# Kernel optimization log

Hardware: AMD Instinct MI355X
Metric: run time of the kernel (lower is better)

Reference implementation:

```python
import jax, jax.numpy as jnp
import numpy as np

G, B, I, H = 512, 64, 32, 64  # num_of_grids, batch, input_size, hidden_size


def setup_inputs() -> dict:
    key = jax.random.key(0)
    ks = jax.random.split(key, 13)
    s = lambda *sh: 1.0 / np.sqrt(sh[-1])
    return {
        "input_data": jax.random.normal(ks[0], (G, B, I), jnp.float32),
        "h0": jax.random.normal(ks[1], (B, H), jnp.float32),
        "c0": jax.random.normal(ks[2], (B, H), jnp.float32),
        # LSTMCell params (torch layout: gates ordered i, f, g, o)
        "W_ih": jax.random.uniform(ks[3], (4 * H, I), jnp.float32, -s(H), s(H)),
        "W_hh": jax.random.uniform(ks[4], (4 * H, H), jnp.float32, -s(H), s(H)),
        "b_ih": jax.random.uniform(ks[5], (4 * H,), jnp.float32, -s(H), s(H)),
        "b_hh": jax.random.uniform(ks[6], (4 * H,), jnp.float32, -s(H), s(H)),
        # MLP head: H*G -> 10*G -> 5*G -> G
        "W1": jax.random.uniform(ks[7], (10 * G, H * G), jnp.float32, -s(H * G), s(H * G)),
        "b1": jax.random.uniform(ks[8], (10 * G,), jnp.float32, -s(H * G), s(H * G)),
        "W2": jax.random.uniform(ks[9], (5 * G, 10 * G), jnp.float32, -s(10 * G), s(10 * G)),
        "b2": jax.random.uniform(ks[10], (5 * G,), jnp.float32, -s(10 * G), s(10 * G)),
        "W3": jax.random.uniform(ks[11], (G, 5 * G), jnp.float32, -s(5 * G), s(5 * G)),
        "b3": jax.random.uniform(ks[12], (G,), jnp.float32, -s(5 * G), s(5 * G)),
    }


def reference(input_data, h0, c0, W_ih, W_hh, b_ih, b_hh, W1, b1, W2, b2, W3, b3):
    def step(carry, x):
        h, c = carry
        gates = x @ W_ih.T + b_ih + h @ W_hh.T + b_hh  # [B, 4H]
        i, f, g, o = jnp.split(gates, 4, axis=-1)
        i, f, o = jax.nn.sigmoid(i), jax.nn.sigmoid(f), jax.nn.sigmoid(o)
        g = jnp.tanh(g)
        c = f * c + i * g
        h = o * jnp.tanh(c)
        return (h, c), h

    _, hs = jax.lax.scan(step, (h0, c0), input_data)  # [G, B, H]
    # torch.cat(list, dim=1) over grid order -> [B, G*H]
    out_all = jnp.transpose(hs, (1, 0, 2)).reshape(h0.shape[0], -1)
    x = out_all @ W1.T + b1
    x = x @ W2.T + b2
    x = x @ W3.T + b3
    return jax.nn.sigmoid(x)  # [B, G]
```

## Files before the change

kernel.cpp:

```cpp
#include <hip/hip_runtime.h>
#include <hip/hip_fp16.h>

#define G_ 512
#define B_ 64
#define I_ 32
#define H_ 64
#define NGATE 256

typedef _Float16 half8 __attribute__((ext_vector_type(8)));
typedef _Float16 h4 __attribute__((ext_vector_type(4)));
typedef _Float16 h2 __attribute__((ext_vector_type(2)));
typedef float f32x4 __attribute__((ext_vector_type(4)));

#if __has_builtin(__builtin_amdgcn_fdot2)
#define FDOT2(a, b, c) __builtin_amdgcn_fdot2((a), (b), (c), false)
#else
#define FDOT2(a, b, c) ((c) + (float)(a)[0] * (float)(b)[0] + (float)(a)[1] * (float)(b)[1])
#endif

__device__ __forceinline__ float sigf(float x) {
  return 1.0f / (1.0f + __expf(-x));
}
__device__ __forceinline__ float tanh_fast(float x) {
  x = fminf(fmaxf(x, -15.0f), 15.0f);
  float e = __expf(2.0f * x);
  return (e - 1.0f) / (e + 1.0f);
}

__global__ __launch_bounds__(256) void k_xproj(
    const float* __restrict__ input, const float* __restrict__ W_ih,
    const float* __restrict__ b_ih, const float* __restrict__ b_hh,
    _Float16* __restrict__ xproj) {
  const int g = blockIdx.x;
  const int t = threadIdx.x;
  const int col = t >> 2;
  const int q = t & 3;
  const int row = q * H_ + col;
  __shared__ alignas(16) float inp[B_ * I_];
  const float* ing = input + (size_t)g * (B_ * I_);
#pragma unroll
  for (int u = 0; u < (B_ * I_) / 256; ++u) inp[u * 256 + t] = ing[u * 256 + t];
  float w[I_];
#pragma unroll
  for (int k = 0; k < I_; k += 4) {
    f32x4 v = *(const f32x4*)(W_ih + (size_t)row * I_ + k);
    w[k] = v[0]; w[k + 1] = v[1]; w[k + 2] = v[2]; w[k + 3] = v[3];
  }
  const float bias = b_ih[row] + b_hh[row];
  __syncthreads();
  for (int b = 0; b < B_; ++b) {
    float a0 = bias, a1 = 0.f, a2 = 0.f, a3 = 0.f;
#pragma unroll
    for (int k = 0; k < I_; k += 4) {
      f32x4 iv = *(const f32x4*)&inp[b * I_ + k];
      a0 += iv[0] * w[k]; a1 += iv[1] * w[k + 1];
      a2 += iv[2] * w[k + 2]; a3 += iv[3] * w[k + 3];
    }
    xproj[((size_t)b * G_ + g) * NGATE + t] = (_Float16)((a0 + a1) + (a2 + a3));
  }
}

__device__ __forceinline__ void scan_row(
    int b, int j, const _Float16* __restrict__ xproj,
    const float* __restrict__ h0, const float* __restrict__ c0,
    const float* __restrict__ W_hh, _Float16* __restrict__ hs,
    _Float16* hsh) {
  h2 w[4][32];
#pragma unroll
  for (int q = 0; q < 4; ++q) {
    const f32x4* wr = (const f32x4*)(W_hh + (size_t)(q * H_ + j) * H_);
#pragma unroll
    for (int kk = 0; kk < 16; ++kk) {
      f32x4 v = wr[kk];
      h2 t0, t1;
      t0[0] = (_Float16)v[0]; t0[1] = (_Float16)v[1];
      t1[0] = (_Float16)v[2]; t1[1] = (_Float16)v[3];
      w[2 * kk & 0 ? 0 : 0][0] = w[0][0];
      w[q][2 * kk] = t0;
      w[q][2 * kk + 1] = t1;
    }
  }
  float c = c0[b * H_ + j];
  hsh[j] = (_Float16)h0[b * H_ + j];

  const h4* xrow = (const h4*)(xproj + (size_t)b * G_ * NGATE) + j;
  h4 p[8];
#pragma unroll
  for (int d = 0; d < 8; ++d) p[d] = xrow[(size_t)d * 64];

  _Float16* hrow = hs + (size_t)b * (G_ * H_) + j;

  for (int g0 = 0; g0 < G_; g0 += 8) {
#pragma unroll
    for (int d = 0; d < 8; ++d) {
      const int g = g0 + d;
      float a[4], a2[4];
#pragma unroll
      for (int q = 0; q < 4; ++q) { a[q] = (float)p[d][q]; a2[q] = 0.0f; }
      const f32x4* hp4 = (const f32x4*)hsh;
#pragma unroll
      for (int k4 = 0; k4 < 4; ++k4) {
        f32x4 hv4 = hp4[k4];
#pragma unroll
        for (int t = 0; t < 4; ++t) {
          h2 hv = __builtin_bit_cast(h2, hv4[t]);
#pragma unroll
          for (int q = 0; q < 4; ++q) a[q] = FDOT2(hv, w[q][k4 * 4 + t], a[q]);
        }
      }
#pragma unroll
      for (int k4 = 4; k4 < 8; ++k4) {
        f32x4 hv4 = hp4[k4];
#pragma unroll
        for (int t = 0; t < 4; ++t) {
          h2 hv = __builtin_bit_cast(h2, hv4[t]);
#pragma unroll
          for (int q = 0; q < 4; ++q) a2[q] = FDOT2(hv, w[q][k4 * 4 + t], a2[q]);
        }
      }
#pragma unroll
      for (int q = 0; q < 4; ++q) a[q] += a2[q];

      float ig = sigf(a[0]);
      float fg = sigf(a[1]);
      float gg = tanh_fast(a[2]);
      float og = sigf(a[3]);
      c = fg * c + ig * gg;
      float hh = og * tanh_fast(c);
      _Float16 hf = (_Float16)hh;
      hsh[j] = hf;
      hrow[(size_t)g * H_] = hf;
      if (g + 8 < G_) p[d] = xrow[(size_t)(g + 8) * 64];
    }
  }
}

__device__ __forceinline__ void conv_loop(
    const float* __restrict__ src, _Float16* __restrict__ dst, int nvec,
    int gtid, int gstride) {
  for (int i = gtid; i < nvec; i += gstride) {
    const f32x4* s = (const f32x4*)(src + (size_t)i * 8);
    f32x4 v0 = s[0];
    f32x4 v1 = s[1];
    half8 h;
    h[0] = (_Float16)v0[0]; h[1] = (_Float16)v0[1];
    h[2] = (_Float16)v0[2]; h[3] = (_Float16)v0[3];
    h[4] = (_Float16)v1[0]; h[5] = (_Float16)v1[1];
    h[6] = (_Float16)v1[2]; h[7] = (_Float16)v1[3];
    *(half8*)(dst + (size_t)i * 8) = h;
  }
}

#define NCONV 2048

__global__ __launch_bounds__(256) void k_scan_conv(
    const _Float16* __restrict__ xproj, const float* __restrict__ h0,
    const float* __restrict__ c0, const float* __restrict__ W_hh,
    _Float16* __restrict__ hs,
    const float* __restrict__ W1, _Float16* __restrict__ W1h,
    const float* __restrict__ W2, _Float16* __restrict__ W2h,
    const float* __restrict__ W3, _Float16* __restrict__ W3h) {
  __shared__ alignas(16) _Float16 hsh[H_];
  const int bid = blockIdx.x;
  if (bid < B_) {
    if (threadIdx.x < 64)
      scan_row(bid, threadIdx.x, xproj, h0, c0, W_hh, hs, hsh);
    return;
  }
  const int gtid = (bid - B_) * 256 + threadIdx.x;
  const int gstride = NCONV * 256;
  conv_loop(W1, W1h, (5120 * 32768) / 8, gtid, gstride);
  conv_loop(W2, W2h, (2560 * 5120) / 8, gtid, gstride);
  conv_loop(W3, W3h, (512 * 2560) / 8, gtid, gstride);
}

template <int N, int K, int KC, int NTILES, int KW>
__global__ __launch_bounds__(256) void k_gemm_h(
    const _Float16* __restrict__ X, const _Float16* __restrict__ Wh,
    float* __restrict__ part) {
  constexpr int ROWB = KW * 2;
  constexpr int SLOTS = ROWB / 16;
  constexpr int RPP = 64 / SLOTS;
  constexpr int NPASS = 16 / RPP;
  static_assert(KC % KW == 0, "stage divisibility");
  __shared__ alignas(16) _Float16 wl[64 * KW];
  const int bid = blockIdx.x;
  const int n0 = (bid % NTILES) * 64;
  const int ks = bid / NTILES;
  const int kbeg = ks * KC;
  const int lane = threadIdx.x & 63;
  const int wave = threadIdx.x >> 6;
  const int r = lane & 15;
  const int gq = lane >> 4;
  const int s = lane % SLOTS;
  const int ro = lane / SLOTS;

  const _Float16* xrow = X + (size_t)r * K + kbeg + 8 * gq;
  f32x4 acc[4] = {};

  for (int st = 0; st < KC / KW; ++st) {
    const int kst = kbeg + st * KW;
#pragma unroll
    for (int pass = 0; pass < NPASS; ++pass) {
      const int rr = wave * 16 + pass * RPP + ro;
      half8 hv = *(const half8*)(Wh + (size_t)(n0 + rr) * K + kst + s * 8);
      int byte = rr * ROWB + s * 16;
      byte ^= (rr & 7) << 4;
      *(half8*)((char*)wl + byte) = hv;
    }
    __syncthreads();
#pragma unroll
    for (int k32 = 0; k32 < KW; k32 += 32) {
      int rbyte = (wave * 16 + r) * ROWB + (k32 + 8 * gq) * 2;
      rbyte ^= (r & 7) << 4;
      half8 bfv = *(const half8*)((const char*)wl + rbyte);
      const _Float16* xp = xrow + st * KW + k32;
#pragma unroll
      for (int mi = 0; mi < 4; ++mi) {
        half8 af = *(const half8*)(xp + (size_t)(mi * 16) * K);
        acc[mi] = __builtin_amdgcn_mfma_f32_16x16x32_f16(af, bfv, acc[mi], 0, 0, 0);
      }
    }
    __syncthreads();
  }
#pragma unroll
  for (int mi = 0; mi < 4; ++mi) {
#pragma unroll
    for (int q = 0; q < 4; ++q) {
      int row = mi * 16 + gq * 4 + q;
      part[((size_t)ks * 64 + row) * N + n0 + wave * 16 + r] = acc[mi][q];
    }
  }
}

template <int N, int KS>
__global__ __launch_bounds__(256) void k_reduce(
    const float* __restrict__ part, const float* __restrict__ bias,
    _Float16* __restrict__ out) {
  const int idx4 = (blockIdx.x * 256 + threadIdx.x) * 4;
  const int n = idx4 % N;
  f32x4 s = *(const f32x4*)(bias + n);
#pragma unroll
  for (int ks = 0; ks < KS; ++ks) s += *(const f32x4*)(part + (size_t)ks * 64 * N + idx4);
#pragma unroll
  for (int t = 0; t < 4; ++t) out[idx4 + t] = (_Float16)s[t];
}

template <int N, int KS>
__global__ __launch_bounds__(256) void k_reduce_sig(
    const float* __restrict__ part, const float* __restrict__ bias,
    float* __restrict__ out) {
  const int idx4 = (blockIdx.x * 256 + threadIdx.x) * 4;
  const int n = idx4 % N;
  f32x4 s = *(const f32x4*)(bias + n);
#pragma unroll
  for (int ks = 0; ks < KS; ++ks) s += *(const f32x4*)(part + (size_t)ks * 64 * N + idx4);
#pragma unroll
  for (int t = 0; t < 4; ++t) out[idx4 + t] = sigf(s[t]);
}

extern "C" void kernel_launch(void* const* d_in, const int* in_sizes, int n_in,
                              void* d_out, int out_size, void* d_ws, size_t ws_size,
                              hipStream_t stream) {
  const float* input = (const float*)d_in[0];
  const float* h0    = (const float*)d_in[1];
  const float* c0    = (const float*)d_in[2];
  const float* W_ih  = (const float*)d_in[3];
  const float* W_hh  = (const float*)d_in[4];
  const float* b_ih  = (const float*)d_in[5];
  const float* b_hh  = (const float*)d_in[6];
  const float* W1    = (const float*)d_in[7];
  const float* b1    = (const float*)d_in[8];
  const float* W2    = (const float*)d_in[9];
  const float* b2    = (const float*)d_in[10];
  const float* W3    = (const float*)d_in[11];
  const float* b3    = (const float*)d_in[12];
  float* out = (float*)d_out;

  uint8_t* ws = (uint8_t*)d_ws;
  float*    part  = (float*)ws;
  _Float16* xproj = (_Float16*)ws;
  _Float16* hs    = (_Float16*)(ws + 41943040);
  _Float16* x2    = (_Float16*)(ws + 46137344);
  _Float16* x3    = (_Float16*)(ws + 46792704);
  _Float16* W1h   = (_Float16*)(ws + 47120384);
  _Float16* W2h   = (_Float16*)(ws + 382664704);
  _Float16* W3h   = (_Float16*)(ws + 408879104);

  k_xproj<<<G_, 256, 0, stream>>>(input, W_ih, b_ih, b_hh, xproj);
  k_scan_conv<<<B_ + NCONV, 256, 0, stream>>>(xproj, h0, c0, W_hh, hs,
                                              W1, W1h, W2, W2h, W3, W3h);
  k_gemm_h<5120, 32768, 1024, 80, 256><<<80 * 32, 256, 0, stream>>>(hs, W1h, part);
  k_reduce<5120, 32><<<(64 * 5120) / 4 / 256, 256, 0, stream>>>(part, b1, x2);
  k_gemm_h<2560, 5120, 640, 40, 128><<<40 * 8, 256, 0, stream>>>(x2, W2h, part);
  k_reduce<2560, 8><<<(64 * 2560) / 4 / 256, 256, 0, stream>>>(part, b2, x3);
  k_gemm_h<512, 2560, 256, 8, 128><<<8 * 10, 256, 0, stream>>>(x3, W3h, part);
  k_reduce_sig<512, 10><<<(64 * 512) / 4 / 256, 256, 0, stream>>>(part, b3, out);
}
```

Measured before the change: 489.6 us.

## Use fp32 packed FMA for LSTM recurrence and shrink scan/convert blocks

The recurrent matvec now keeps W_hh and the shared hidden state in fp32 and uses packed fp32 FMA (v_pk_fma_f32) in place of fp16 fdot2. The fused scan/convert kernel also drops from 256 to 64 threads per block, so scan blocks no longer carry 192 idle lanes, and launch bounds are set to (64,1) to allow more registers. The number of conversion blocks falls from 2048 to 768. This removes fp16 conversions on the serial critical path, but it doubles the weight register footprint, and the fewer, smaller conversion blocks may convert the weights more slowly.

```diff
diff --git a/kernel.cpp b/kernel.cpp
--- a/kernel.cpp
+++ b/kernel.cpp
@@ -9,13 +9,18 @@
 
 typedef _Float16 half8 __attribute__((ext_vector_type(8)));
 typedef _Float16 h4 __attribute__((ext_vector_type(4)));
-typedef _Float16 h2 __attribute__((ext_vector_type(2)));
 typedef float f32x4 __attribute__((ext_vector_type(4)));
-
-#if __has_builtin(__builtin_amdgcn_fdot2)
-#define FDOT2(a, b, c) __builtin_amdgcn_fdot2((a), (b), (c), false)
+typedef float f32x2 __attribute__((ext_vector_type(2)));
+
+#if __has_builtin(__builtin_elementwise_fma)
+#define PKFMA(a, b, c) __builtin_elementwise_fma((a), (b), (c))
 #else
-#define FDOT2(a, b, c) ((c) + (float)(a)[0] * (float)(b)[0] + (float)(a)[1] * (float)(b)[1])
+__device__ __forceinline__ f32x2 PKFMA(f32x2 a, f32x2 b, f32x2 c) {
+  f32x2 r;
+  r[0] = __builtin_fmaf(a[0], b[0], c[0]);
+  r[1] = __builtin_fmaf(a[1], b[1], c[1]);
+  return r;
+}
 #endif
 
 __device__ __forceinline__ float sigf(float x) {
@@ -64,24 +69,20 @@
     int b, int j, const _Float16* __restrict__ xproj,
     const float* __restrict__ h0, const float* __restrict__ c0,
     const float* __restrict__ W_hh, _Float16* __restrict__ hs,
-    _Float16* hsh) {
-  h2 w[4][32];
+    float* hsh) {
+  f32x2 w[4][32];
 #pragma unroll
   for (int q = 0; q < 4; ++q) {
     const f32x4* wr = (const f32x4*)(W_hh + (size_t)(q * H_ + j) * H_);
 #pragma unroll
     for (int kk = 0; kk < 16; ++kk) {
       f32x4 v = wr[kk];
-      h2 t0, t1;
-      t0[0] = (_Float16)v[0]; t0[1] = (_Float16)v[1];
-      t1[0] = (_Float16)v[2]; t1[1] = (_Float16)v[3];
-      w[2 * kk & 0 ? 0 : 0][0] = w[0][0];
-      w[q][2 * kk] = t0;
-      w[q][2 * kk + 1] = t1;
+      w[q][2 * kk] = f32x2{v[0], v[1]};
+      w[q][2 * kk + 1] = f32x2{v[2], v[3]};
     }
   }
   float c = c0[b * H_ + j];
-  hsh[j] = (_Float16)h0[b * H_ + j];
+  hsh[j] = h0[b * H_ + j];
 
   const h4* xrow = (const h4*)(xproj + (size_t)b * G_ * NGATE) + j;
   h4 p[8];
@@ -94,42 +95,50 @@
 #pragma unroll
     for (int d = 0; d < 8; ++d) {
       const int g = g0 + d;
-      float a[4], a2[4];
-#pragma unroll
-      for (int q = 0; q < 4; ++q) { a[q] = (float)p[d][q]; a2[q] = 0.0f; }
+      f32x2 a[4], a2[4];
+#pragma unroll
+      for (int q = 0; q < 4; ++q) {
+        a[q] = f32x2{(float)p[d][q], 0.0f};
+        a2[q] = f32x2{0.0f, 0.0f};
+      }
       const f32x4* hp4 = (const f32x4*)hsh;
 #pragma unroll
-      for (int k4 = 0; k4 < 4; ++k4) {
-        f32x4 hv4 = hp4[k4];
-#pragma unroll
-        for (int t = 0; t < 4; ++t) {
-          h2 hv = __builtin_bit_cast(h2, hv4[t]);
-#pragma unroll
-          for (int q = 0; q < 4; ++q) a[q] = FDOT2(hv, w[q][k4 * 4 + t], a[q]);
+      for (int k4 = 0; k4 < 8; ++k4) {
+        f32x4 hv = hp4[k4];
+        f32x2 lo = f32x2{hv[0], hv[1]};
+        f32x2 hi = f32x2{hv[2], hv[3]};
+#pragma unroll
+        for (int q = 0; q < 4; ++q) {
+          a[q] = PKFMA(w[q][2 * k4], lo, a[q]);
+          a2[q] = PKFMA(w[q][2 * k4 + 1], hi, a2[q]);
         }
       }
 #pragma unroll
-      for (int k4 = 4; k4 < 8; ++k4) {
-        f32x4 hv4 = hp4[k4];
-#pragma unroll
-        for (int t = 0; t < 4; ++t) {
-          h2 hv = __builtin_bit_cast(h2, hv4[t]);
-#pragma unroll
-          for (int q = 0; q < 4; ++q) a2[q] = FDOT2(hv, w[q][k4 * 4 + t], a2[q]);
+      for (int k4 = 8; k4 < 16; ++k4) {
+        f32x4 hv = hp4[k4];
+        f32x2 lo = f32x2{hv[0], hv[1]};
+        f32x2 hi = f32x2{hv[2], hv[3]};
+#pragma unroll
+        for (int q = 0; q < 4; ++q) {
+          a[q] = PKFMA(w[q][2 * k4], lo, a[q]);
+          a2[q] = PKFMA(w[q][2 * k4 + 1], hi, a2[q]);
         }
       }
-#pragma unroll
-      for (int q = 0; q < 4; ++q) a[q] += a2[q];
-
-      float ig = sigf(a[0]);
-      float fg = sigf(a[1]);
-      float gg = tanh_fast(a[2]);
-      float og = sigf(a[3]);
+      float gate[4];
+#pragma unroll
+      for (int q = 0; q < 4; ++q) {
+        f32x2 s = a[q] + a2[q];
+        gate[q] = s[0] + s[1];
+      }
+
+      float ig = sigf(gate[0]);
+      float fg = sigf(gate[1]);
+      float gg = tanh_fast(gate[2]);
+      float og = sigf(gate[3]);
       c = fg * c + ig * gg;
       float hh = og * tanh_fast(c);
-      _Float16 hf = (_Float16)hh;
-      hsh[j] = hf;
-      hrow[(size_t)g * H_] = hf;
+      hsh[j] = hh;
+      hrow[(size_t)g * H_] = (_Float16)hh;
       if (g + 8 < G_) p[d] = xrow[(size_t)(g + 8) * 64];
     }
   }
@@ -151,24 +160,23 @@
   }
 }
 
-#define NCONV 2048
-
-__global__ __launch_bounds__(256) void k_scan_conv(
+#define NCONV 768
+
+__global__ __launch_bounds__(64, 1) void k_scan_conv(
     const _Float16* __restrict__ xproj, const float* __restrict__ h0,
     const float* __restrict__ c0, const float* __restrict__ W_hh,
     _Float16* __restrict__ hs,
     const float* __restrict__ W1, _Float16* __restrict__ W1h,
     const float* __restrict__ W2, _Float16* __restrict__ W2h,
     const float* __restrict__ W3, _Float16* __restrict__ W3h) {
-  __shared__ alignas(16) _Float16 hsh[H_];
+  __shared__ alignas(16) float hsh[H_];
   const int bid = blockIdx.x;
   if (bid < B_) {
-    if (threadIdx.x < 64)
-      scan_row(bid, threadIdx.x, xproj, h0, c0, W_hh, hs, hsh);
+    scan_row(bid, threadIdx.x, xproj, h0, c0, W_hh, hs, hsh);
     return;
   }
-  const int gtid = (bid - B_) * 256 + threadIdx.x;
-  const int gstride = NCONV * 256;
+  const int gtid = (bid - B_) * 64 + threadIdx.x;
+  const int gstride = NCONV * 64;
   conv_loop(W1, W1h, (5120 * 32768) / 8, gtid, gstride);
   conv_loop(W2, W2h, (2560 * 5120) / 8, gtid, gstride);
   conv_loop(W3, W3h, (512 * 2560) / 8, gtid, gstride);
@@ -288,8 +296,8 @@
   _Float16* W3h   = (_Float16*)(ws + 408879104);
 
   k_xproj<<<G_, 256, 0, stream>>>(input, W_ih, b_ih, b_hh, xproj);
-  k_scan_conv<<<B_ + NCONV, 256, 0, stream>>>(xproj, h0, c0, W_hh, hs,
-                                              W1, W1h, W2, W2h, W3, W3h);
+  k_scan_conv<<<B_ + NCONV, 64, 0, stream>>>(xproj, h0, c0, W_hh, hs,
+                                             W1, W1h, W2, W2h, W3, W3h);
   k_gemm_h<5120, 32768, 1024, 80, 256><<<80 * 32, 256, 0, stream>>>(hs, W1h, part);
   k_reduce<5120, 32><<<(64 * 5120) / 4 / 256, 256, 0, stream>>>(part, b1, x2);
   k_gemm_h<2560, 5120, 640, 40, 128><<<40 * 8, 256, 0, stream>>>(x2, W2h, part);
```

Measured after the change: 697.2 us. 42.4% more time.

## Pre-tile swizzled fp16 weights and stream tiles via direct global-to-LDS loads

Applied to the files above, without the earlier changes.

The fp32-to-fp16 weight conversion now writes each weight matrix in 64-row by KW-column tiles, already XOR-swizzled into the exact LDS layout the GEMM uses. The GEMM kernels then copy each tile contiguously with global_load_lds 16-byte transfers instead of strided per-row vector loads followed by register-to-LDS stores. This removes the VGPR round-trip and gives each wave fully coalesced contiguous reads. In exchange the conversion kernel does more index arithmetic and its stores are scattered, and the GEMM layout is now tied to the tiling chosen at conversion time.

```diff
diff --git a/kernel.cpp b/kernel.cpp
--- a/kernel.cpp
+++ b/kernel.cpp
@@ -25,6 +25,12 @@
   x = fminf(fmaxf(x, -15.0f), 15.0f);
   float e = __expf(2.0f * x);
   return (e - 1.0f) / (e + 1.0f);
+}
+
+__device__ __forceinline__ void gload_lds16(const _Float16* g, _Float16* l) {
+  __builtin_amdgcn_global_load_lds(
+      (const __attribute__((address_space(1))) void*)g,
+      (__attribute__((address_space(3))) void*)l, 16, 0, 0);
 }
 
 __global__ __launch_bounds__(256) void k_xproj(
@@ -75,7 +81,6 @@
       h2 t0, t1;
       t0[0] = (_Float16)v[0]; t0[1] = (_Float16)v[1];
       t1[0] = (_Float16)v[2]; t1[1] = (_Float16)v[3];
-      w[2 * kk & 0 ? 0 : 0][0] = w[0][0];
       w[q][2 * kk] = t0;
       w[q][2 * kk + 1] = t1;
     }
@@ -135,11 +140,16 @@
   }
 }
 
-__device__ __forceinline__ void conv_loop(
-    const float* __restrict__ src, _Float16* __restrict__ dst, int nvec,
+template <int N, int K, int KWT>
+__device__ __forceinline__ void conv_tiled(
+    const float* __restrict__ src, _Float16* __restrict__ dst,
     int gtid, int gstride) {
-  for (int i = gtid; i < nvec; i += gstride) {
-    const f32x4* s = (const f32x4*)(src + (size_t)i * 8);
+  constexpr int ROWB = KWT * 2;
+  constexpr int TILEH = 64 * KWT;
+  for (int i = gtid; i < N * (K / 8); i += gstride) {
+    const int n = i / (K / 8);
+    const int k8 = i % (K / 8);
+    const f32x4* s = (const f32x4*)(src + (size_t)n * K + (size_t)k8 * 8);
     f32x4 v0 = s[0];
     f32x4 v1 = s[1];
     half8 h;
@@ -147,7 +157,12 @@
     h[2] = (_Float16)v0[2]; h[3] = (_Float16)v0[3];
     h[4] = (_Float16)v1[0]; h[5] = (_Float16)v1[1];
     h[6] = (_Float16)v1[2]; h[7] = (_Float16)v1[3];
-    *(half8*)(dst + (size_t)i * 8) = h;
+    const int nt = n >> 6, rr = n & 63;
+    const int ksg = k8 / (KWT / 8);
+    const int kk8 = k8 % (KWT / 8);
+    const size_t tile_id = (size_t)nt * (K / KWT) + ksg;
+    int byte = rr * ROWB + ((kk8 * 16) ^ ((rr & 7) << 4));
+    *(half8*)((char*)(dst + tile_id * TILEH) + byte) = h;
   }
 }
 
@@ -169,44 +184,41 @@
   }
   const int gtid = (bid - B_) * 256 + threadIdx.x;
   const int gstride = NCONV * 256;
-  conv_loop(W1, W1h, (5120 * 32768) / 8, gtid, gstride);
-  conv_loop(W2, W2h, (2560 * 5120) / 8, gtid, gstride);
-  conv_loop(W3, W3h, (512 * 2560) / 8, gtid, gstride);
+  conv_tiled<5120, 32768, 256>(W1, W1h, gtid, gstride);
+  conv_tiled<2560, 5120, 128>(W2, W2h, gtid, gstride);
+  conv_tiled<512, 2560, 128>(W3, W3h, gtid, gstride);
 }
 
 template <int N, int K, int KC, int NTILES, int KW>
-__global__ __launch_bounds__(256) void k_gemm_h(
+__global__ __launch_bounds__(256) void k_gemm_t(
     const _Float16* __restrict__ X, const _Float16* __restrict__ Wh,
     float* __restrict__ part) {
   constexpr int ROWB = KW * 2;
-  constexpr int SLOTS = ROWB / 16;
-  constexpr int RPP = 64 / SLOTS;
-  constexpr int NPASS = 16 / RPP;
+  constexpr int TILEB = 64 * ROWB;
+  constexpr int WBYTES = TILEB / 4;
+  constexpr int CALLS = WBYTES / 1024;
   static_assert(KC % KW == 0, "stage divisibility");
-  __shared__ alignas(16) _Float16 wl[64 * KW];
+  __shared__ alignas(16) _Float16 wl[TILEB / 2];
   const int bid = blockIdx.x;
-  const int n0 = (bid % NTILES) * 64;
+  const int nt = bid % NTILES;
   const int ks = bid / NTILES;
+  const int n0 = nt * 64;
   const int kbeg = ks * KC;
   const int lane = threadIdx.x & 63;
   const int wave = threadIdx.x >> 6;
   const int r = lane & 15;
   const int gq = lane >> 4;
-  const int s = lane % SLOTS;
-  const int ro = lane / SLOTS;
 
   const _Float16* xrow = X + (size_t)r * K + kbeg + 8 * gq;
   f32x4 acc[4] = {};
 
   for (int st = 0; st < KC / KW; ++st) {
-    const int kst = kbeg + st * KW;
-#pragma unroll
-    for (int pass = 0; pass < NPASS; ++pass) {
-      const int rr = wave * 16 + pass * RPP + ro;
-      half8 hv = *(const half8*)(Wh + (size_t)(n0 + rr) * K + kst + s * 8);
-      int byte = rr * ROWB + s * 16;
-      byte ^= (rr & 7) << 4;
-      *(half8*)((char*)wl + byte) = hv;
+    const size_t tile_id = (size_t)nt * (K / KW) + (size_t)(kbeg / KW) + st;
+    const _Float16* tile = Wh + tile_id * (TILEB / 2);
+#pragma unroll
+    for (int c = 0; c < CALLS; ++c) {
+      const int uoff_h = (wave * WBYTES + c * 1024) / 2;
+      gload_lds16(tile + uoff_h + lane * 8, wl + uoff_h);
     }
     __syncthreads();
 #pragma unroll
@@ -290,10 +302,10 @@
   k_xproj<<<G_, 256, 0, stream>>>(input, W_ih, b_ih, b_hh, xproj);
   k_scan_conv<<<B_ + NCONV, 256, 0, stream>>>(xproj, h0, c0, W_hh, hs,
                                               W1, W1h, W2, W2h, W3, W3h);
-  k_gemm_h<5120, 32768, 1024, 80, 256><<<80 * 32, 256, 0, stream>>>(hs, W1h, part);
+  k_gemm_t<5120, 32768, 1024, 80, 256><<<80 * 32, 256, 0, stream>>>(hs, W1h, part);
   k_reduce<5120, 32><<<(64 * 5120) / 4 / 256, 256, 0, stream>>>(part, b1, x2);
-  k_gemm_h<2560, 5120, 640, 40, 128><<<40 * 8, 256, 0, stream>>>(x2, W2h, part);
+  k_gemm_t<2560, 5120, 640, 40, 128><<<40 * 8, 256, 0, stream>>>(x2, W2h, part);
   k_reduce<2560, 8><<<(64 * 2560) / 4 / 256, 256, 0, stream>>>(part, b2, x3);
-  k_gemm_h<512, 2560, 256, 8, 128><<<8 * 10, 256, 0, stream>>>(x3, W3h, part);
+  k_gemm_t<512, 2560, 256, 8, 128><<<8 * 10, 256, 0, stream>>>(x3, W3h, part);
   k_reduce_sig<512, 10><<<(64 * 512) / 4 / 256, 256, 0, stream>>>(part, b3, out);
 }
```

Measured after the change: 497.6 us. No clear change (+1.6%).
